# Performance work log

Hardware: AMD Instinct MI355X
Metric: run time of the kernel (lower is better)

## Reference

```python
import jax, jax.numpy as jnp
import numpy as np

DIM = 32
BATCH = 131072
NH = 100

def _init_linear(key, nin, nout):
    k1, k2 = jax.random.split(key)
    bound = 1.0 / np.sqrt(nin)
    W = jax.random.uniform(k1, (nin, nout), minval=-bound, maxval=bound, dtype=jnp.float32)
    b = jax.random.uniform(k2, (nout,), minval=-bound, maxval=bound, dtype=jnp.float32)
    return W, b

def setup_inputs() -> dict:
    key = jax.random.key(0)
    ks = jax.random.split(key, 8)
    e = jax.random.normal(ks[0], (BATCH, DIM), dtype=jnp.float32)
    # causal adjacency: strictly upper-triangular random 0/1 (parents j of node i satisfy j < i)
    Craw = jax.random.bernoulli(ks[1], 0.5, (DIM, DIM)).astype(jnp.float32)
    C = Craw * jnp.triu(jnp.ones((DIM, DIM), jnp.float32), k=1)
    s_W1, s_b1 = _init_linear(ks[2], DIM, NH)
    s_W2, s_b2 = _init_linear(ks[3], NH, NH)
    s_W3, s_b3 = _init_linear(ks[4], NH, 1)
    t_W1, t_b1 = _init_linear(ks[5], DIM, NH)
    t_W2, t_b2 = _init_linear(ks[6], NH, NH)
    t_W3, t_b3 = _init_linear(ks[7], NH, 1)
    return {"e": e, "C": C,
            "s_W1": s_W1, "s_b1": s_b1, "s_W2": s_W2, "s_b2": s_b2, "s_W3": s_W3, "s_b3": s_b3,
            "t_W1": t_W1, "t_b1": t_b1, "t_W2": t_W2, "t_b2": t_b2, "t_W3": t_W3, "t_b3": t_b3}

def _mlp(x, W1, b1, W2, b2, W3, b3):
    # linear -> relu -> linear -> relu -> linear -> sigmoid, squeeze last dim
    h = jax.nn.relu(x @ W1 + b1)
    h = jax.nn.relu(h @ W2 + b2)
    return jax.nn.sigmoid(h @ W3 + b3)[:, 0]  # [B]

def reference(e, C, s_W1, s_b1, s_W2, s_b2, s_W3, s_b3, t_W1, t_b1, t_W2, t_b2, t_W3, t_b3):
    B, dim = e.shape

    def step(carry, xs):
        z, log_det = carry
        i, mask, e_i = xs          # mask = C[:, i] (all-zero column == zero mask branch in torch)
        x = z * mask               # [B, dim]
        s = _mlp(x, s_W1, s_b1, s_W2, s_b2, s_W3, s_b3)
        t = _mlp(x, t_W1, t_b1, t_W2, t_b2, t_W3, t_b3)
        z = z.at[:, i].set(jnp.exp(s) * e_i + t)
        return (z, log_det + s), None

    init = (jnp.zeros_like(e), jnp.zeros((B,), e.dtype))
    (z, log_det), _ = jax.lax.scan(step, init, (jnp.arange(dim), C.T, e.T))
    return z, log_det
```

## Files before the change

### kernel.cpp

```cpp
#include <hip/hip_runtime.h>


typedef __attribute__((ext_vector_type(8))) short short8;
typedef __attribute__((ext_vector_type(4))) float f32x4;
typedef __attribute__((ext_vector_type(4))) unsigned int uint4v;

#define WPK_U16 39936
#define MPK_OFF_BYTES 79872
#define NBLK 2048
#define REPS 4

__device__ __forceinline__ unsigned int bf16u(float v) {
  unsigned int b = __float_as_uint(v);
  b += 0x7FFFu + ((b >> 16) & 1u);
  return b >> 16;
}

__device__ __forceinline__ unsigned int cvtpk(float lo, float hi) {
  unsigned int r;
  asm("v_cvt_pk_bf16_f32 %0, %1, %2" : "=v"(r) : "v"(lo), "v"(hi));
  return r;
}

__device__ __forceinline__ unsigned int pkrelu(unsigned int x) {
  unsigned int r;
  asm("v_pk_max_i16 %0, %1, %2" : "=v"(r) : "v"(x), "v"(0u));
  return r;
}

__device__ __forceinline__ void pack_h(const f32x4 (&h)[7], uint4v (&B)[4],
                                       bool g1) {
#pragma unroll
  for (int c = 0; c < 3; ++c) {
    B[c].x = pkrelu(cvtpk(h[2 * c][0], h[2 * c][1]));
    B[c].y = pkrelu(cvtpk(h[2 * c][2], h[2 * c][3]));
    B[c].z = pkrelu(cvtpk(h[2 * c + 1][0], h[2 * c + 1][1]));
    B[c].w = pkrelu(cvtpk(h[2 * c + 1][2], h[2 * c + 1][3]));
  }
  float v0 = g1 ? 1.0f : h[6][0];
  B[3].x = pkrelu(cvtpk(v0, h[6][1]));
  B[3].y = pkrelu(cvtpk(h[6][2], h[6][3]));
  B[3].z = 0u;
  B[3].w = 0u;
}

__device__ __forceinline__ void mlp2_eval(
    const short8 (&a1s)[7], const short8 (&a2s)[7][4], const short8 (&a3s)[4],
    const short8 (&a1t)[7], const short8 (&a2t)[7][4], const short8 (&a3t)[4],
    short8 x, bool g1, float &sp, float &tp) {
  const f32x4 zz = {0.f, 0.f, 0.f, 0.f};
  f32x4 h1s[7], h1t[7];
#pragma unroll
  for (int t = 0; t < 7; ++t) {
    h1s[t] = __builtin_amdgcn_mfma_f32_16x16x32_bf16(a1s[t], x, zz, 0, 0, 0);
    h1t[t] = __builtin_amdgcn_mfma_f32_16x16x32_bf16(a1t[t], x, zz, 0, 0, 0);
  }
  uint4v B1s[4], B1t[4];
  pack_h(h1s, B1s, g1);
  pack_h(h1t, B1t, g1);
  f32x4 h2s[7], h2t[7];
#pragma unroll
  for (int t = 0; t < 7; ++t) { h2s[t] = zz; h2t[t] = zz; }
#pragma unroll
  for (int c = 0; c < 4; ++c) {
    short8 Bs = __builtin_bit_cast(short8, B1s[c]);
    short8 Bt = __builtin_bit_cast(short8, B1t[c]);
#pragma unroll
    for (int t = 0; t < 7; ++t) {
      h2s[t] = __builtin_amdgcn_mfma_f32_16x16x32_bf16(a2s[t][c], Bs, h2s[t], 0, 0, 0);
      h2t[t] = __builtin_amdgcn_mfma_f32_16x16x32_bf16(a2t[t][c], Bt, h2t[t], 0, 0, 0);
    }
  }
  uint4v B2s[4], B2t[4];
  pack_h(h2s, B2s, g1);
  pack_h(h2t, B2t, g1);
  f32x4 as0 = __builtin_amdgcn_mfma_f32_16x16x32_bf16(a3s[0], __builtin_bit_cast(short8, B2s[0]), zz, 0, 0, 0);
  f32x4 at0 = __builtin_amdgcn_mfma_f32_16x16x32_bf16(a3t[0], __builtin_bit_cast(short8, B2t[0]), zz, 0, 0, 0);
  f32x4 as1 = __builtin_amdgcn_mfma_f32_16x16x32_bf16(a3s[1], __builtin_bit_cast(short8, B2s[1]), zz, 0, 0, 0);
  f32x4 at1 = __builtin_amdgcn_mfma_f32_16x16x32_bf16(a3t[1], __builtin_bit_cast(short8, B2t[1]), zz, 0, 0, 0);
  f32x4 as2 = __builtin_amdgcn_mfma_f32_16x16x32_bf16(a3s[2], __builtin_bit_cast(short8, B2s[2]), zz, 0, 0, 0);
  f32x4 at2 = __builtin_amdgcn_mfma_f32_16x16x32_bf16(a3t[2], __builtin_bit_cast(short8, B2t[2]), zz, 0, 0, 0);
  f32x4 as3 = __builtin_amdgcn_mfma_f32_16x16x32_bf16(a3s[3], __builtin_bit_cast(short8, B2s[3]), zz, 0, 0, 0);
  f32x4 at3 = __builtin_amdgcn_mfma_f32_16x16x32_bf16(a3t[3], __builtin_bit_cast(short8, B2t[3]), zz, 0, 0, 0);
  sp = (as0[0] + as1[0]) + (as2[0] + as3[0]);
  tp = (at0[0] + at1[0]) + (at2[0] + at3[0]);
}

__global__ void prepack_kernel(const float *__restrict__ C,
                               const float *__restrict__ sW1, const float *__restrict__ sb1,
                               const float *__restrict__ sW2, const float *__restrict__ sb2,
                               const float *__restrict__ sW3, const float *__restrict__ sb3,
                               const float *__restrict__ tW1, const float *__restrict__ tb1,
                               const float *__restrict__ tW2, const float *__restrict__ tb2,
                               const float *__restrict__ tW3, const float *__restrict__ tb3,
                               unsigned short *__restrict__ wpk,
                               unsigned int *__restrict__ mpk) {
  int gid = blockIdx.x * 256 + threadIdx.x;
  if (gid < WPK_U16) {
    int which = gid / 19968;
    int a = gid % 19968;
    const float *W1 = which ? tW1 : sW1;
    const float *B1 = which ? tb1 : sb1;
    const float *W2 = which ? tW2 : sW2;
    const float *B2 = which ? tb2 : sb2;
    const float *W3 = which ? tW3 : sW3;
    const float *B3 = which ? tb3 : sb3;
    float v = 0.f;
    if (a < 3584) {
      int t = a >> 9; int rem = a & 511; int l = rem >> 3; int j = rem & 7;
      int m = 16 * t + (l & 15);
      int d = 8 * (l >> 4) + j;
      if (m < 100) {
        if (d == 31) v = B1[m];
        else v = W1[d * 100 + m];
      }
    } else if (a < 17920) {
      int b = a - 3584; int tc = b >> 9; int t = tc >> 2; int c = tc & 3;
      int rem = b & 511; int l = rem >> 3; int j = rem & 7;
      int m = 16 * t + (l & 15);
      int k = 32 * c + (j >> 2) * 16 + 4 * (l >> 4) + (j & 3);
      if (m < 100) {
        if (k < 100) v = W2[k * 100 + m];
        else if (k == 100) v = B2[m];
      }
    } else {
      int b = a - 17920; int c = b >> 9; int rem = b & 511;
      int l = rem >> 3; int j = rem & 7;
      int k = 32 * c + (j >> 2) * 16 + 4 * (l >> 4) + (j & 3);
      (void)l;
      if (k < 100) v = W3[k];
      else if (k == 100) v = B3[0];
    }
    wpk[gid] = (unsigned short)bf16u(v);
  } else if (gid < WPK_U16 + 512) {
    int idx = gid - WPK_U16;
    int i = idx >> 4;
    int G = (idx >> 2) & 3;
    int p = idx & 3;
    int d0 = 8 * G + 2 * p;
    unsigned int u = 0;
    if (C[d0 * 32 + i] != 0.f) u |= 0x0000FFFFu;
    if (C[(d0 + 1) * 32 + i] != 0.f) u |= 0xFFFF0000u;
    mpk[idx] = u;
  }
}

__global__ __launch_bounds__(64, 1) void flow_main(
    const float *__restrict__ e, const unsigned short *__restrict__ wpk,
    const unsigned int *__restrict__ mpk, float *__restrict__ out) {
  const int lane = threadIdx.x;
  const int G = lane >> 4;
  const int bl = lane & 15;
  const bool g1 = (G == 1);
  const bool g3 = (G == 3);

  __shared__ __align__(16) unsigned int msk[512];
  {
    const uint4v *s = (const uint4v *)mpk;
    uint4v *d = (uint4v *)msk;
    d[lane] = s[lane];
    d[lane + 64] = s[lane + 64];
  }

  const short8 *w = (const short8 *)wpk;
  short8 a1s[7], a2s[7][4], a3s[4];
  short8 a1t[7], a2t[7][4], a3t[4];
#pragma unroll
  for (int t = 0; t < 7; ++t) a1s[t] = w[t * 64 + lane];
#pragma unroll
  for (int t = 0; t < 7; ++t)
#pragma unroll
    for (int c = 0; c < 4; ++c) a2s[t][c] = w[448 + (t * 4 + c) * 64 + lane];
#pragma unroll
  for (int c = 0; c < 4; ++c) a3s[c] = w[2240 + c * 64 + lane];
#pragma unroll
  for (int t = 0; t < 7; ++t) a1t[t] = w[2496 + t * 64 + lane];
#pragma unroll
  for (int t = 0; t < 7; ++t)
#pragma unroll
    for (int c = 0; c < 4; ++c)
      a2t[t][c] = w[2496 + 448 + (t * 4 + c) * 64 + lane];
#pragma unroll
  for (int c = 0; c < 4; ++c) a3t[c] = w[2496 + 2240 + c * 64 + lane];

#pragma unroll
  for (int t = 0; t < 7; ++t)
#pragma unroll
    for (int c = 0; c < 4; ++c) {
      asm volatile("" : "+a"(a2s[t][c]));
      asm volatile("" : "+a"(a2t[t][c]));
    }
#pragma unroll
  for (int c = 0; c < 4; ++c) {
    asm volatile("" : "+a"(a3s[c]));
    asm volatile("" : "+a"(a3t[c]));
  }

#pragma unroll 1
  for (int rep = 0; rep < REPS; ++rep) {
    const long base = ((long)blockIdx.x * REPS + rep) * 16;
    const float *ep = e + (base + bl) * 32 + G * 8;
    f32x4 e0 = *(const f32x4 *)ep;
    f32x4 e1 = *(const f32x4 *)(ep + 4);
    unsigned int z0 = 0, z1 = 0, z2 = 0, z3 = 0;
    float ld = 0.f;
    uint4v m = *(const uint4v *)&msk[G * 4];

#pragma unroll 1
    for (int i8 = 0; i8 < 4; ++i8) {
      const bool tg = (G == i8);
#pragma unroll
      for (int u = 0; u < 8; ++u) {
        const int i = i8 * 8 + u;
        uint4v mn = *(const uint4v *)&msk[((i + 1) & 31) * 16 + G * 4];
        unsigned int x0 = z0 & m.x, x1 = z1 & m.y, x2 = z2 & m.z, x3 = z3 & m.w;
        if (g3) x3 = (x3 & 0x0000FFFFu) | 0x3F800000u;
        uint4v xu; xu.x = x0; xu.y = x1; xu.z = x2; xu.w = x3;
        short8 x = __builtin_bit_cast(short8, xu);

        float sp, tp;
        mlp2_eval(a1s, a2s, a3s, a1t, a2t, a3t, x, g1, sp, tp);
        float sv = __fdividef(1.f, 1.f + __expf(-sp));
        float tv = __fdividef(1.f, 1.f + __expf(-tp));
        ld += sv;

        float es = (u < 4) ? e0[u] : e1[u - 4];
        float zn = __expf(sv) * es + tv;
        unsigned int r = cvtpk(zn, zn);
        const int p = (u >> 1) & 3;
        const bool hi = (u & 1) != 0;
        unsigned int mrg;
        if (p == 0) {
          mrg = hi ? ((z0 & 0x0000FFFFu) | (r & 0xFFFF0000u))
                   : ((z0 & 0xFFFF0000u) | (r & 0x0000FFFFu));
          z0 = tg ? mrg : z0;
        } else if (p == 1) {
          mrg = hi ? ((z1 & 0x0000FFFFu) | (r & 0xFFFF0000u))
                   : ((z1 & 0xFFFF0000u) | (r & 0x0000FFFFu));
          z1 = tg ? mrg : z1;
        } else if (p == 2) {
          mrg = hi ? ((z2 & 0x0000FFFFu) | (r & 0xFFFF0000u))
                   : ((z2 & 0xFFFF0000u) | (r & 0x0000FFFFu));
          z2 = tg ? mrg : z2;
        } else {
          mrg = hi ? ((z3 & 0x0000FFFFu) | (r & 0xFFFF0000u))
                   : ((z3 & 0xFFFF0000u) | (r & 0x0000FFFFu));
          z3 = tg ? mrg : z3;
        }
        m = mn;
      }
    }

    float *zo = out + (base + bl) * 32 + G * 8;
    f32x4 o0, o1;
    o0[0] = __uint_as_float(z0 << 16);
    o0[1] = __uint_as_float(z0 & 0xFFFF0000u);
    o0[2] = __uint_as_float(z1 << 16);
    o0[3] = __uint_as_float(z1 & 0xFFFF0000u);
    o1[0] = __uint_as_float(z2 << 16);
    o1[1] = __uint_as_float(z2 & 0xFFFF0000u);
    o1[2] = __uint_as_float(z3 << 16);
    o1[3] = __uint_as_float(z3 & 0xFFFF0000u);
    *(f32x4 *)zo = o0;
    *(f32x4 *)(zo + 4) = o1;
    if (lane < 16) out[(long)131072 * 32 + base + bl] = ld;
  }
}

extern "C" void kernel_launch(void *const *d_in, const int *in_sizes, int n_in,
                              void *d_out, int out_size, void *d_ws, size_t ws_size,
                              hipStream_t stream) {
  const float *e  = (const float *)d_in[0];
  const float *C  = (const float *)d_in[1];
  const float *sW1 = (const float *)d_in[2];
  const float *sb1 = (const float *)d_in[3];
  const float *sW2 = (const float *)d_in[4];
  const float *sb2 = (const float *)d_in[5];
  const float *sW3 = (const float *)d_in[6];
  const float *sb3 = (const float *)d_in[7];
  const float *tW1 = (const float *)d_in[8];
  const float *tb1 = (const float *)d_in[9];
  const float *tW2 = (const float *)d_in[10];
  const float *tb2 = (const float *)d_in[11];
  const float *tW3 = (const float *)d_in[12];
  const float *tb3 = (const float *)d_in[13];

  unsigned short *wpk = (unsigned short *)d_ws;
  unsigned int *mpk = (unsigned int *)((char *)d_ws + MPK_OFF_BYTES);
  float *out = (float *)d_out;

  prepack_kernel<<<dim3(159), dim3(256), 0, stream>>>(
      C, sW1, sb1, sW2, sb2, sW3, sb3, tW1, tb1, tW2, tb2, tW3, tb3, wpk, mpk);
  flow_main<<<dim3(NBLK), dim3(64), 0, stream>>>(e, wpk, mpk, out);
}
```

Before: 270.5 us.

## Interleave two independent 16-row batches per wave to hide MFMA dependency latency

Each wave now processes two 16-row tiles (A and B) at the same time instead of one tile per iteration, halving the outer rep loop. The per-step chain of dependent MFMA layers is serial, so a second independent tile gives the scheduler more work to overlap its latency. The e values are now read per step from global/L1 instead of being preloaded into registers. The MLP helper is split so the s and t networks run separately, and the first layer-2 accumulation starts from the first product instead of a zero-accumulate. Register pressure rises with two z states and more live accumulators, which could cause spills.

```diff
diff --git a/kernel.cpp b/kernel.cpp
--- a/kernel.cpp
+++ b/kernel.cpp
@@ -8,7 +8,6 @@
 #define WPK_U16 39936
 #define MPK_OFF_BYTES 79872
 #define NBLK 2048
-#define REPS 4
 
 __device__ __forceinline__ unsigned int bf16u(float v) {
   unsigned int b = __float_as_uint(v);
@@ -44,46 +43,38 @@
   B[3].w = 0u;
 }
 
-__device__ __forceinline__ void mlp2_eval(
-    const short8 (&a1s)[7], const short8 (&a2s)[7][4], const short8 (&a3s)[4],
-    const short8 (&a1t)[7], const short8 (&a2t)[7][4], const short8 (&a3t)[4],
-    short8 x, bool g1, float &sp, float &tp) {
+__device__ __forceinline__ float mlp_eval(const short8 (&a1)[7],
+                                          const short8 (&a2)[7][4],
+                                          const short8 (&a3)[4],
+                                          short8 x, bool g1) {
   const f32x4 zz = {0.f, 0.f, 0.f, 0.f};
-  f32x4 h1s[7], h1t[7];
-#pragma unroll
-  for (int t = 0; t < 7; ++t) {
-    h1s[t] = __builtin_amdgcn_mfma_f32_16x16x32_bf16(a1s[t], x, zz, 0, 0, 0);
-    h1t[t] = __builtin_amdgcn_mfma_f32_16x16x32_bf16(a1t[t], x, zz, 0, 0, 0);
-  }
-  uint4v B1s[4], B1t[4];
-  pack_h(h1s, B1s, g1);
-  pack_h(h1t, B1t, g1);
-  f32x4 h2s[7], h2t[7];
-#pragma unroll
-  for (int t = 0; t < 7; ++t) { h2s[t] = zz; h2t[t] = zz; }
-#pragma unroll
-  for (int c = 0; c < 4; ++c) {
-    short8 Bs = __builtin_bit_cast(short8, B1s[c]);
-    short8 Bt = __builtin_bit_cast(short8, B1t[c]);
-#pragma unroll
-    for (int t = 0; t < 7; ++t) {
-      h2s[t] = __builtin_amdgcn_mfma_f32_16x16x32_bf16(a2s[t][c], Bs, h2s[t], 0, 0, 0);
-      h2t[t] = __builtin_amdgcn_mfma_f32_16x16x32_bf16(a2t[t][c], Bt, h2t[t], 0, 0, 0);
-    }
-  }
-  uint4v B2s[4], B2t[4];
-  pack_h(h2s, B2s, g1);
-  pack_h(h2t, B2t, g1);
-  f32x4 as0 = __builtin_amdgcn_mfma_f32_16x16x32_bf16(a3s[0], __builtin_bit_cast(short8, B2s[0]), zz, 0, 0, 0);
-  f32x4 at0 = __builtin_amdgcn_mfma_f32_16x16x32_bf16(a3t[0], __builtin_bit_cast(short8, B2t[0]), zz, 0, 0, 0);
-  f32x4 as1 = __builtin_amdgcn_mfma_f32_16x16x32_bf16(a3s[1], __builtin_bit_cast(short8, B2s[1]), zz, 0, 0, 0);
-  f32x4 at1 = __builtin_amdgcn_mfma_f32_16x16x32_bf16(a3t[1], __builtin_bit_cast(short8, B2t[1]), zz, 0, 0, 0);
-  f32x4 as2 = __builtin_amdgcn_mfma_f32_16x16x32_bf16(a3s[2], __builtin_bit_cast(short8, B2s[2]), zz, 0, 0, 0);
-  f32x4 at2 = __builtin_amdgcn_mfma_f32_16x16x32_bf16(a3t[2], __builtin_bit_cast(short8, B2t[2]), zz, 0, 0, 0);
-  f32x4 as3 = __builtin_amdgcn_mfma_f32_16x16x32_bf16(a3s[3], __builtin_bit_cast(short8, B2s[3]), zz, 0, 0, 0);
-  f32x4 at3 = __builtin_amdgcn_mfma_f32_16x16x32_bf16(a3t[3], __builtin_bit_cast(short8, B2t[3]), zz, 0, 0, 0);
-  sp = (as0[0] + as1[0]) + (as2[0] + as3[0]);
-  tp = (at0[0] + at1[0]) + (at2[0] + at3[0]);
+  f32x4 h1[7];
+#pragma unroll
+  for (int t = 0; t < 7; ++t)
+    h1[t] = __builtin_amdgcn_mfma_f32_16x16x32_bf16(a1[t], x, zz, 0, 0, 0);
+  uint4v B1[4];
+  pack_h(h1, B1, g1);
+  f32x4 h2[7];
+  {
+    short8 B0 = __builtin_bit_cast(short8, B1[0]);
+#pragma unroll
+    for (int t = 0; t < 7; ++t)
+      h2[t] = __builtin_amdgcn_mfma_f32_16x16x32_bf16(a2[t][0], B0, zz, 0, 0, 0);
+  }
+#pragma unroll
+  for (int c = 1; c < 4; ++c) {
+    short8 B = __builtin_bit_cast(short8, B1[c]);
+#pragma unroll
+    for (int t = 0; t < 7; ++t)
+      h2[t] = __builtin_amdgcn_mfma_f32_16x16x32_bf16(a2[t][c], B, h2[t], 0, 0, 0);
+  }
+  uint4v B2[4];
+  pack_h(h2, B2, g1);
+  f32x4 a0 = __builtin_amdgcn_mfma_f32_16x16x32_bf16(a3[0], __builtin_bit_cast(short8, B2[0]), zz, 0, 0, 0);
+  f32x4 a1r = __builtin_amdgcn_mfma_f32_16x16x32_bf16(a3[1], __builtin_bit_cast(short8, B2[1]), zz, 0, 0, 0);
+  f32x4 a2r = __builtin_amdgcn_mfma_f32_16x16x32_bf16(a3[2], __builtin_bit_cast(short8, B2[2]), zz, 0, 0, 0);
+  f32x4 a3r = __builtin_amdgcn_mfma_f32_16x16x32_bf16(a3[3], __builtin_bit_cast(short8, B2[3]), zz, 0, 0, 0);
+  return (a0[0] + a1r[0]) + (a2r[0] + a3r[0]);
 }
 
 __global__ void prepack_kernel(const float *__restrict__ C,
@@ -197,13 +188,14 @@
   }
 
 #pragma unroll 1
-  for (int rep = 0; rep < REPS; ++rep) {
-    const long base = ((long)blockIdx.x * REPS + rep) * 16;
-    const float *ep = e + (base + bl) * 32 + G * 8;
-    f32x4 e0 = *(const f32x4 *)ep;
-    f32x4 e1 = *(const f32x4 *)(ep + 4);
-    unsigned int z0 = 0, z1 = 0, z2 = 0, z3 = 0;
-    float ld = 0.f;
+  for (int rp = 0; rp < 2; ++rp) {
+    const long baseA = ((long)blockIdx.x * 4 + rp * 2) * 16;
+    const long baseB = baseA + 16;
+    const float *erowA = e + (baseA + bl) * 32;
+    const float *erowB = e + (baseB + bl) * 32;
+    unsigned int zA0 = 0, zA1 = 0, zA2 = 0, zA3 = 0;
+    unsigned int zB0 = 0, zB1 = 0, zB2 = 0, zB3 = 0;
+    float ldA = 0.f, ldB = 0.f;
     uint4v m = *(const uint4v *)&msk[G * 4];
 
 #pragma unroll 1
@@ -212,58 +204,99 @@
 #pragma unroll
       for (int u = 0; u < 8; ++u) {
         const int i = i8 * 8 + u;
+        float esA = erowA[i];
+        float esB = erowB[i];
         uint4v mn = *(const uint4v *)&msk[((i + 1) & 31) * 16 + G * 4];
-        unsigned int x0 = z0 & m.x, x1 = z1 & m.y, x2 = z2 & m.z, x3 = z3 & m.w;
-        if (g3) x3 = (x3 & 0x0000FFFFu) | 0x3F800000u;
-        uint4v xu; xu.x = x0; xu.y = x1; xu.z = x2; xu.w = x3;
-        short8 x = __builtin_bit_cast(short8, xu);
-
-        float sp, tp;
-        mlp2_eval(a1s, a2s, a3s, a1t, a2t, a3t, x, g1, sp, tp);
-        float sv = __fdividef(1.f, 1.f + __expf(-sp));
-        float tv = __fdividef(1.f, 1.f + __expf(-tp));
-        ld += sv;
-
-        float es = (u < 4) ? e0[u] : e1[u - 4];
-        float zn = __expf(sv) * es + tv;
-        unsigned int r = cvtpk(zn, zn);
+
+        uint4v xa, xb;
+        xa.x = zA0 & m.x; xa.y = zA1 & m.y; xa.z = zA2 & m.z; xa.w = zA3 & m.w;
+        xb.x = zB0 & m.x; xb.y = zB1 & m.y; xb.z = zB2 & m.z; xb.w = zB3 & m.w;
+        if (g3) {
+          xa.w = (xa.w & 0x0000FFFFu) | 0x3F800000u;
+          xb.w = (xb.w & 0x0000FFFFu) | 0x3F800000u;
+        }
+        short8 xA = __builtin_bit_cast(short8, xa);
+        short8 xB = __builtin_bit_cast(short8, xb);
+
+        float spA = mlp_eval(a1s, a2s, a3s, xA, g1);
+        float spB = mlp_eval(a1s, a2s, a3s, xB, g1);
+        float tpA = mlp_eval(a1t, a2t, a3t, xA, g1);
+        float tpB = mlp_eval(a1t, a2t, a3t, xB, g1);
+
+        float svA = __fdividef(1.f, 1.f + __expf(-spA));
+        float tvA = __fdividef(1.f, 1.f + __expf(-tpA));
+        float svB = __fdividef(1.f, 1.f + __expf(-spB));
+        float tvB = __fdividef(1.f, 1.f + __expf(-tpB));
+        ldA += svA;
+        ldB += svB;
+
+        float znA = __expf(svA) * esA + tvA;
+        float znB = __expf(svB) * esB + tvB;
+        unsigned int rA = cvtpk(znA, znA);
+        unsigned int rB = cvtpk(znB, znB);
         const int p = (u >> 1) & 3;
         const bool hi = (u & 1) != 0;
-        unsigned int mrg;
+        unsigned int mg;
         if (p == 0) {
-          mrg = hi ? ((z0 & 0x0000FFFFu) | (r & 0xFFFF0000u))
-                   : ((z0 & 0xFFFF0000u) | (r & 0x0000FFFFu));
-          z0 = tg ? mrg : z0;
+          mg = hi ? ((zA0 & 0x0000FFFFu) | (rA & 0xFFFF0000u))
+                  : ((zA0 & 0xFFFF0000u) | (rA & 0x0000FFFFu));
+          zA0 = tg ? mg : zA0;
+          mg = hi ? ((zB0 & 0x0000FFFFu) | (rB & 0xFFFF0000u))
+                  : ((zB0 & 0xFFFF0000u) | (rB & 0x0000FFFFu));
+          zB0 = tg ? mg : zB0;
         } else if (p == 1) {
-          mrg = hi ? ((z1 & 0x0000FFFFu) | (r & 0xFFFF0000u))
-                   : ((z1 & 0xFFFF0000u) | (r & 0x0000FFFFu));
-          z1 = tg ? mrg : z1;
+          mg = hi ? ((zA1 & 0x0000FFFFu) | (rA & 0xFFFF0000u))
+                  : ((zA1 & 0xFFFF0000u) | (rA & 0x0000FFFFu));
+          zA1 = tg ? mg : zA1;
+          mg = hi ? ((zB1 & 0x0000FFFFu) | (rB & 0xFFFF0000u))
+                  : ((zB1 & 0xFFFF0000u) | (rB & 0x0000FFFFu));
+          zB1 = tg ? mg : zB1;
         } else if (p == 2) {
-          mrg = hi ? ((z2 & 0x0000FFFFu) | (r & 0xFFFF0000u))
-                   : ((z2 & 0xFFFF0000u) | (r & 0x0000FFFFu));
-          z2 = tg ? mrg : z2;
+          mg = hi ? ((zA2 & 0x0000FFFFu) | (rA & 0xFFFF0000u))
+                  : ((zA2 & 0xFFFF0000u) | (rA & 0x0000FFFFu));
+          zA2 = tg ? mg : zA2;
+          mg = hi ? ((zB2 & 0x0000FFFFu) | (rB & 0xFFFF0000u))
+                  : ((zB2 & 0xFFFF0000u) | (rB & 0x0000FFFFu));
+          zB2 = tg ? mg : zB2;
         } else {
-          mrg = hi ? ((z3 & 0x0000FFFFu) | (r & 0xFFFF0000u))
-                   : ((z3 & 0xFFFF0000u) | (r & 0x0000FFFFu));
-          z3 = tg ? mrg : z3;
+          mg = hi ? ((zA3 & 0x0000FFFFu) | (rA & 0xFFFF0000u))
+                  : ((zA3 & 0xFFFF0000u) | (rA & 0x0000FFFFu));
+          zA3 = tg ? mg : zA3;
+          mg = hi ? ((zB3 & 0x0000FFFFu) | (rB & 0xFFFF0000u))
+                  : ((zB3 & 0xFFFF0000u) | (rB & 0x0000FFFFu));
+          zB3 = tg ? mg : zB3;
         }
         m = mn;
       }
     }
 
-    float *zo = out + (base + bl) * 32 + G * 8;
-    f32x4 o0, o1;
-    o0[0] = __uint_as_float(z0 << 16);
-    o0[1] = __uint_as_float(z0 & 0xFFFF0000u);
-    o0[2] = __uint_as_float(z1 << 16);
-    o0[3] = __uint_as_float(z1 & 0xFFFF0000u);
-    o1[0] = __uint_as_float(z2 << 16);
-    o1[1] = __uint_as_float(z2 & 0xFFFF0000u);
-    o1[2] = __uint_as_float(z3 << 16);
-    o1[3] = __uint_as_float(z3 & 0xFFFF0000u);
-    *(f32x4 *)zo = o0;
-    *(f32x4 *)(zo + 4) = o1;
-    if (lane < 16) out[(long)131072 * 32 + base + bl] = ld;
+    float *zoA = out + (baseA + bl) * 32 + G * 8;
+    float *zoB = out + (baseB + bl) * 32 + G * 8;
+    f32x4 o;
+    o[0] = __uint_as_float(zA0 << 16);
+    o[1] = __uint_as_float(zA0 & 0xFFFF0000u);
+    o[2] = __uint_as_float(zA1 << 16);
+    o[3] = __uint_as_float(zA1 & 0xFFFF0000u);
+    *(f32x4 *)zoA = o;
+    o[0] = __uint_as_float(zA2 << 16);
+    o[1] = __uint_as_float(zA2 & 0xFFFF0000u);
+    o[2] = __uint_as_float(zA3 << 16);
+    o[3] = __uint_as_float(zA3 & 0xFFFF0000u);
+    *(f32x4 *)(zoA + 4) = o;
+    o[0] = __uint_as_float(zB0 << 16);
+    o[1] = __uint_as_float(zB0 & 0xFFFF0000u);
+    o[2] = __uint_as_float(zB1 << 16);
+    o[3] = __uint_as_float(zB1 & 0xFFFF0000u);
+    *(f32x4 *)zoB = o;
+    o[0] = __uint_as_float(zB2 << 16);
+    o[1] = __uint_as_float(zB2 & 0xFFFF0000u);
+    o[2] = __uint_as_float(zB3 << 16);
+    o[3] = __uint_as_float(zB3 & 0xFFFF0000u);
+    *(f32x4 *)(zoB + 4) = o;
+    if (lane < 16) {
+      out[(long)131072 * 32 + baseA + bl] = ldA;
+      out[(long)131072 * 32 + baseB + bl] = ldB;
+    }
   }
 }
 
```

After: 301.9 us. 11.6% more time.
